# Kernel optimization log

Hardware: AMD Instinct MI355X
Metric: run time of the kernel (lower is better)

## Reference

```python
import jax, jax.numpy as jnp
import numpy as np
from jax import lax

K = 3  # kernel size
KK = K * K


def _bilinear_gather(img, ys, xs):
    """img: [C, H, W]; ys, xs: [KK, H, W] float sample coords.
    Returns [C, KK, H, W], zero outside the image (torch DCN zero-pad semantics)."""
    C, H, W = img.shape
    y0 = jnp.floor(ys).astype(jnp.int32)
    x0 = jnp.floor(xs).astype(jnp.int32)
    y1, x1 = y0 + 1, x0 + 1
    wy1 = ys - y0.astype(ys.dtype)
    wx1 = xs - x0.astype(xs.dtype)
    wy0, wx0 = 1.0 - wy1, 1.0 - wx1

    def g(yi, xi):
        valid = ((yi >= 0) & (yi < H) & (xi >= 0) & (xi < W)).astype(img.dtype)
        yc = jnp.clip(yi, 0, H - 1)
        xc = jnp.clip(xi, 0, W - 1)
        return img[:, yc, xc] * valid[None]  # [C, KK, H, W]

    return (wy0 * wx0) * g(y0, x0) + (wy0 * wx1) * g(y0, x1) \
         + (wy1 * wx0) * g(y1, x0) + (wy1 * wx1) * g(y1, x1)


def _df_layer(x, w_off, b_off, w):
    """One DFConv2d (modulated DCN, k=3, s=1, d=1, pad=1, groups=1) + ReLU."""
    B, C, H, W = x.shape
    O = w.shape[0]
    # offset/mask conv (standard 3x3, pad 1, with bias)
    om = lax.conv_general_dilated(x, w_off, (1, 1), [(1, 1), (1, 1)],
                                  dimension_numbers=('NCHW', 'OIHW', 'NCHW'))
    om = om + b_off[None, :, None, None]                     # [B, 27, H, W]
    off = om[:, :2 * KK].reshape(B, KK, 2, H, W)             # (dy, dx) per kernel pt
    mask = jax.nn.sigmoid(om[:, 2 * KK:3 * KK])              # [B, KK, H, W]

    ki, kj = jnp.meshgrid(jnp.arange(K), jnp.arange(K), indexing='ij')
    # base sampling grid: y = h - pad + i*dil = h + i - 1
    base_y = jnp.arange(H, dtype=x.dtype)[None, :, None] + (ki.reshape(KK, 1, 1).astype(x.dtype) - 1.0)
    base_x = jnp.arange(W, dtype=x.dtype)[None, None, :] + (kj.reshape(KK, 1, 1).astype(x.dtype) - 1.0)
    ys = base_y + off[:, :, 0]                               # [B, KK, H, W]
    xs = base_x + off[:, :, 1]

    sampled = jax.vmap(_bilinear_gather)(x, ys, xs)          # [B, C, KK, H, W]
    out = jnp.einsum('oik,bikhw->bohw', w.reshape(O, C, KK), sampled * mask[:, None])
    return jax.nn.relu(out)


def setup_inputs() -> dict:
    key = jax.random.key(0)
    ks = jax.random.split(key, 7)
    s = 0.05
    return {
        'x': jax.random.normal(ks[0], (2, 256, 96, 96), dtype=jnp.float32),
        'w_off0': jax.random.normal(ks[1], (27, 256, 3, 3), dtype=jnp.float32) * s,
        'b_off0': jnp.zeros((27,), dtype=jnp.float32),
        'w0': jax.random.normal(ks[2], (256, 256, 3, 3), dtype=jnp.float32) * s,
        'w_off1': jax.random.normal(ks[3], (27, 256, 3, 3), dtype=jnp.float32) * s,
        'b_off1': jnp.zeros((27,), dtype=jnp.float32),
        'w1': jax.random.normal(ks[4], (256, 256, 3, 3), dtype=jnp.float32) * s,
    }


def reference(x, w_off0, b_off0, w0, w_off1, b_off1, w1):
    h = _df_layer(x, w_off0, b_off0, w0)
    h = _df_layer(h, w_off1, b_off1, w1)
    return h
```

## Files before the change

### kernel.cpp

```cpp
#include <hip/hip_runtime.h>
#include <cstdint>
#include <cstddef>


#define KTOT 2304
#define PXB  9216

typedef __attribute__((ext_vector_type(8))) short bf16x8;
typedef __attribute__((ext_vector_type(4))) float f32x4;

static __device__ __forceinline__ unsigned short f2bf(float f) {
    union { float f; unsigned int u; } v; v.f = f;
    unsigned int r = (v.u + 0x7FFFu + ((v.u >> 16) & 1u)) >> 16;
    return (unsigned short)r;
}
static __device__ __forceinline__ float bf2f(unsigned short h) {
    union { unsigned int u; float f; } v; v.u = ((unsigned int)h) << 16;
    return v.f;
}
static __device__ __forceinline__ void unpack8(uint4 u, float* f) {
    union { unsigned int u; float f; } t;
    t.u = u.x << 16;         f[0] = t.f;
    t.u = u.x & 0xffff0000u; f[1] = t.f;
    t.u = u.y << 16;         f[2] = t.f;
    t.u = u.y & 0xffff0000u; f[3] = t.f;
    t.u = u.z << 16;         f[4] = t.f;
    t.u = u.z & 0xffff0000u; f[5] = t.f;
    t.u = u.w << 16;         f[6] = t.f;
    t.u = u.w & 0xffff0000u; f[7] = t.f;
}

__global__ __launch_bounds__(256) void transpose_kernel(const float* __restrict__ in,
                                                        unsigned short* __restrict__ outH,
                                                        unsigned short* __restrict__ outL) {
    __shared__ float tile[64][65];
    const int hw0 = blockIdx.x * 64;
    const int c0  = blockIdx.y * 64;
    const int b   = blockIdx.z;
    const int lx  = threadIdx.x & 63;
    const int ly  = threadIdx.x >> 6;
#pragma unroll
    for (int i = 0; i < 16; ++i) {
        int cl = ly + i * 4;
        tile[cl][lx] = in[(size_t)(b * 256 + c0 + cl) * PXB + hw0 + lx];
    }
    __syncthreads();
#pragma unroll
    for (int i = 0; i < 16; ++i) {
        int hwl = ly + i * 4;
        float v = tile[lx][hwl];
        size_t oi = ((size_t)b * PXB + hw0 + hwl) * 256 + c0 + lx;
        unsigned short hi = f2bf(v);
        outH[oi] = hi;
        outL[oi] = f2bf(v - bf2f(hi));
    }
}

__global__ __launch_bounds__(256) void prep_w_kernel(const float* __restrict__ w,
                                                     unsigned short* __restrict__ wA) {
    int idx = blockIdx.x * 256 + threadIdx.x;
    int o = idx / KTOT;
    int k = idx - o * KTOT;
    int kk = k >> 8;
    int c  = k & 255;
    wA[idx] = f2bf(w[o * KTOT + c * 9 + kk]);
}

__global__ __launch_bounds__(256) void prep_woff_kernel(const float* __restrict__ w,
                                                        unsigned short* __restrict__ wH,
                                                        unsigned short* __restrict__ wL) {
    int idx = blockIdx.x * 256 + threadIdx.x;
    int o = idx / KTOT;
    int k = idx - o * KTOT;
    int kk = k >> 8;
    int c  = k & 255;
    float f = (o < 27) ? w[o * KTOT + c * 9 + kk] : 0.0f;
    unsigned short hi = f2bf(f);
    wH[idx] = hi;
    wL[idx] = f2bf(f - bf2f(hi));
}

__global__ __launch_bounds__(512) void offconv_fused(const unsigned short* __restrict__ xH,
                                                     const unsigned short* __restrict__ xL,
                                                     const unsigned short* __restrict__ AH,
                                                     const unsigned short* __restrict__ AL,
                                                     const float* __restrict__ bias,
                                                     float* __restrict__ om) {
    __shared__ __attribute__((aligned(16))) unsigned short AsH[2][32 * 72];
    __shared__ __attribute__((aligned(16))) unsigned short AsL[2][32 * 72];
    __shared__ __attribute__((aligned(16))) unsigned short BsH[2][64 * 72];
    __shared__ __attribute__((aligned(16))) unsigned short BsL[2][64 * 72];

    const int tid  = threadIdx.x;
    const int kg   = tid >> 8;
    const int tl   = tid & 255;
    const int lane = tid & 63;
    const int wq   = (tid >> 6) & 3;
    const int quad = lane >> 4, l16 = lane & 15;
    const int g    = blockIdx.x;
    const int nb   = (g & 7) * 36 + (g >> 3);
    const int n0   = nb * 64;
    const int b    = n0 / PXB;
    const int hw0  = n0 - b * PXB;

    f32x4 acc[2];
#pragma unroll
    for (int mt = 0; mt < 2; ++mt) acc[mt] = (f32x4)0.0f;

    const int arow = tl >> 3, akg = tl & 7;

    uint4 pAH, pAL, pBH0, pBL0, pBH1, pBL1;
    auto pf = [&](int it) {
        const int kt = kg * 18 + it;
        const int kk = kt >> 2, c0 = (kt & 3) * 64;
        const int dy = kk / 3 - 1, dx = kk - (kk / 3) * 3 - 1;
        size_t ai = (size_t)arow * KTOT + kt * 64 + akg * 8;
        pAH = *(const uint4*)&AH[ai];
        pAL = *(const uint4*)&AL[ai];
#pragma unroll
        for (int i = 0; i < 2; ++i) {
            int task = i * 256 + tl;
            int px = task >> 3, cg = task & 7;
            int hw = hw0 + px;
            int h = hw / 96, w = hw - h * 96;
            int y = h + dy, x = w + dx;
            uint4 hv = make_uint4(0u, 0u, 0u, 0u), lv = make_uint4(0u, 0u, 0u, 0u);
            if (((unsigned)y < 96u) && ((unsigned)x < 96u)) {
                size_t bi = ((size_t)b * PXB + y * 96 + x) * 256 + c0 + cg * 8;
                hv = *(const uint4*)&xH[bi];
                lv = *(const uint4*)&xL[bi];
            }
            if (i == 0) { pBH0 = hv; pBL0 = lv; } else { pBH1 = hv; pBL1 = lv; }
        }
    };
    pf(0);

    for (int it = 0; it < 18; ++it) {
        __syncthreads();
        *(uint4*)&AsH[kg][arow * 72 + akg * 8] = pAH;
        *(uint4*)&AsL[kg][arow * 72 + akg * 8] = pAL;
        {
            int px = tl >> 3, cg = tl & 7;
            *(uint4*)&BsH[kg][px * 72 + cg * 8] = pBH0;
            *(uint4*)&BsL[kg][px * 72 + cg * 8] = pBL0;
        }
        {
            int task = 256 + tl;
            int px = task >> 3, cg = task & 7;
            *(uint4*)&BsH[kg][px * 72 + cg * 8] = pBH1;
            *(uint4*)&BsL[kg][px * 72 + cg * 8] = pBL1;
        }
        if (it < 17) pf(it + 1);
        __syncthreads();
#pragma unroll
        for (int ks = 0; ks < 2; ++ks) {
            bf16x8 ah[2], al[2], bh, bl;
#pragma unroll
            for (int mt = 0; mt < 2; ++mt) {
                ah[mt] = *(const bf16x8*)&AsH[kg][(mt * 16 + l16) * 72 + ks * 32 + quad * 8];
                al[mt] = *(const bf16x8*)&AsL[kg][(mt * 16 + l16) * 72 + ks * 32 + quad * 8];
            }
            bh = *(const bf16x8*)&BsH[kg][(wq * 16 + l16) * 72 + ks * 32 + quad * 8];
            bl = *(const bf16x8*)&BsL[kg][(wq * 16 + l16) * 72 + ks * 32 + quad * 8];
#pragma unroll
            for (int mt = 0; mt < 2; ++mt) {
                acc[mt] = __builtin_amdgcn_mfma_f32_16x16x32_bf16(ah[mt], bh, acc[mt], 0, 0, 0);
                acc[mt] = __builtin_amdgcn_mfma_f32_16x16x32_bf16(ah[mt], bl, acc[mt], 0, 0, 0);
                acc[mt] = __builtin_amdgcn_mfma_f32_16x16x32_bf16(al[mt], bh, acc[mt], 0, 0, 0);
            }
        }
    }

    float* red = (float*)BsH;
    __syncthreads();
    if (kg == 1) {
#pragma unroll
        for (int mt = 0; mt < 2; ++mt)
#pragma unroll
            for (int r = 0; r < 4; ++r)
                red[wq * 512 + mt * 256 + quad * 64 + r * 16 + l16] = acc[mt][r];
    }
    __syncthreads();
    if (kg == 0) {
#pragma unroll
        for (int mt = 0; mt < 2; ++mt)
#pragma unroll
            for (int r = 0; r < 4; ++r) {
                float v = acc[mt][r] + red[wq * 512 + mt * 256 + quad * 64 + r * 16 + l16];
                int m = mt * 16 + quad * 4 + r;
                int n = wq * 16 + l16;
                if (m < 27)
                    om[(size_t)(b * 27 + m) * PXB + hw0 + n] = v + bias[m];
            }
    }
}

__global__ __launch_bounds__(512, 4) void dfconv_v2(const unsigned short* __restrict__ xB,
                                                    const float* __restrict__ om,
                                                    const unsigned short* __restrict__ A,
                                                    float* __restrict__ out,
                                                    unsigned short* __restrict__ outH,
                                                    unsigned short* __restrict__ outL,
                                                    int out_mode) {
    __shared__ __attribute__((aligned(16))) char smem[81664];
    unsigned short* Bbuf0 = (unsigned short*)(smem + 65536);
    unsigned short* Bbuf1 = (unsigned short*)(smem + 70144);
    unsigned short* goff  = (unsigned short*)(smem + 74752);
    float*          gwt   = (float*)(smem + 77056);

    const int tid  = threadIdx.x;
    const int wv   = tid >> 6;
    const int lane = tid & 63;
    const int quad = lane >> 4, l16 = lane & 15;
    const int g    = blockIdx.x;
    const int nb   = (g & 7) * 72 + (g >> 3);
    const int n0   = nb * 32;
    const int b    = n0 / PXB;
    const int hw0  = n0 - b * PXB;

    if (tid < 288) {
        int task = tid;
        int px = task / 9;
        int kk = task - px * 9;
        int hw = hw0 + px;
        int h = hw / 96, w = hw - h * 96;
        const float* omp = om + (size_t)b * 27 * PXB + hw;
        float dyv = omp[(size_t)(2 * kk) * PXB];
        float dxv = omp[(size_t)(2 * kk + 1) * PXB];
        float mv  = omp[(size_t)(18 + kk) * PXB];
        float mk  = 1.0f / (1.0f + __expf(-mv));

        float ys = (float)(h + (kk / 3) - 1) + dyv;
        float xs = (float)(w + (kk - (kk / 3) * 3) - 1) + dxv;
        float fy = floorf(ys), fx = floorf(xs);
        int iy = (int)fy, ix = (int)fx;
        float wy1 = ys - fy, wx1 = xs - fx;
        float wy0 = 1.0f - wy1, wx0 = 1.0f - wx1;
        bool yv0 = (unsigned)iy < 96u, yv1 = (unsigned)(iy + 1) < 96u;
        bool xv0 = (unsigned)ix < 96u, xv1 = (unsigned)(ix + 1) < 96u;
        int y0 = min(max(iy, 0), 95),     y1 = min(max(iy + 1, 0), 95);
        int x0 = min(max(ix, 0), 95),     x1 = min(max(ix + 1, 0), 95);
        int gg = task * 4;
        goff[gg + 0] = (unsigned short)(y0 * 96 + x0);
        goff[gg + 1] = (unsigned short)(y0 * 96 + x1);
        goff[gg + 2] = (unsigned short)(y1 * 96 + x0);
        goff[gg + 3] = (unsigned short)(y1 * 96 + x1);
        gwt[gg + 0] = (yv0 && xv0) ? mk * wy0 * wx0 : 0.0f;
        gwt[gg + 1] = (yv0 && xv1) ? mk * wy0 * wx1 : 0.0f;
        gwt[gg + 2] = (yv1 && xv0) ? mk * wy1 * wx0 : 0.0f;
        gwt[gg + 3] = (yv1 && xv1) ? mk * wy1 * wx1 : 0.0f;
    }
    __syncthreads();

    const int px = (tid & 255) >> 3;
    const int cg = tid & 7;
    const unsigned short* xbase = xB + (size_t)b * PXB * 256 + cg * 8;

    const int arl = lane >> 3;
    const int akg = (lane & 7) ^ arl;

    f32x4 acc[2][2];
#pragma unroll
    for (int mt = 0; mt < 2; ++mt)
#pragma unroll
        for (int nt = 0; nt < 2; ++nt) acc[mt][nt] = (f32x4)0.0f;

    auto dmaA = [&](int kt, int buf) {
#pragma unroll
        for (int s = 0; s < 4; ++s) {
            const unsigned short* src =
                A + (size_t)(wv * 32 + s * 8 + arl) * KTOT + kt * 64 + akg * 8;
            char* dst = smem + buf * 32768 + wv * 4096 + s * 1024;
            __builtin_amdgcn_global_load_lds(
                (const __attribute__((address_space(1))) unsigned int*)src,
                (__attribute__((address_space(3))) unsigned int*)dst, 16, 0, 0);
        }
    };

    dmaA(0, 0);
    if (tid < 256) {
        int gg = (px * 9 + 0) * 4;
        ushort4 o4 = *(const ushort4*)&goff[gg];
        float4 wt = *(const float4*)&gwt[gg];
        uint4 u0 = *(const uint4*)(xbase + (size_t)o4.x * 256);
        uint4 u1 = *(const uint4*)(xbase + (size_t)o4.y * 256);
        uint4 u2 = *(const uint4*)(xbase + (size_t)o4.z * 256);
        uint4 u3 = *(const uint4*)(xbase + (size_t)o4.w * 256);
        float f0[8], f1[8], f2[8], f3[8];
        unpack8(u0, f0); unpack8(u1, f1); unpack8(u2, f2); unpack8(u3, f3);
        unsigned short res[8];
#pragma unroll
        for (int j = 0; j < 8; ++j)
            res[j] = f2bf(wt.x * f0[j] + wt.y * f1[j] + wt.z * f2[j] + wt.w * f3[j]);
        *(uint4*)&Bbuf0[px * 72 + cg * 8] = *(uint4*)res;
    }
    __syncthreads();

    for (int r = 0; r < 36; ++r) {
        const int cur = r & 1;

        uint4 cc0, cc1, cc2, cc3; float4 wt;
        if (tid < 256 && r < 35) {
            const int ktn = r + 1, tap = ktn >> 2, c0 = (ktn & 3) * 64;
            int gg = (px * 9 + tap) * 4;
            ushort4 o4 = *(const ushort4*)&goff[gg];
            wt = *(const float4*)&gwt[gg];
            const unsigned short* cb = xbase + c0;
            cc0 = *(const uint4*)(cb + (size_t)o4.x * 256);
            cc1 = *(const uint4*)(cb + (size_t)o4.y * 256);
            cc2 = *(const uint4*)(cb + (size_t)o4.z * 256);
            cc3 = *(const uint4*)(cb + (size_t)o4.w * 256);
        }

        if (r < 35) dmaA(r + 1, cur ^ 1);

        {
            const char* Ac = smem + cur * 32768 + wv * 4096;
            const unsigned short* Br = cur ? Bbuf1 : Bbuf0;
#pragma unroll
            for (int ks = 0; ks < 2; ++ks) {
                const int sw = (((ks * 4 + quad) ^ (l16 & 7)) * 16);
                bf16x8 a0 = *(const bf16x8*)(Ac + l16 * 128 + sw);
                bf16x8 a1 = *(const bf16x8*)(Ac + (16 + l16) * 128 + sw);
                bf16x8 b0 = *(const bf16x8*)&Br[l16 * 72 + ks * 32 + quad * 8];
                bf16x8 b1 = *(const bf16x8*)&Br[(16 + l16) * 72 + ks * 32 + quad * 8];
                acc[0][0] = __builtin_amdgcn_mfma_f32_16x16x32_bf16(a0, b0, acc[0][0], 0, 0, 0);
                acc[0][1] = __builtin_amdgcn_mfma_f32_16x16x32_bf16(a0, b1, acc[0][1], 0, 0, 0);
                acc[1][0] = __builtin_amdgcn_mfma_f32_16x16x32_bf16(a1, b0, acc[1][0], 0, 0, 0);
                acc[1][1] = __builtin_amdgcn_mfma_f32_16x16x32_bf16(a1, b1, acc[1][1], 0, 0, 0);
            }
        }

        if (tid < 256 && r < 35) {
            unsigned short* Bw = cur ? Bbuf0 : Bbuf1;
            float f0[8], f1[8], f2[8], f3[8];
            unpack8(cc0, f0); unpack8(cc1, f1); unpack8(cc2, f2); unpack8(cc3, f3);
            unsigned short res[8];
#pragma unroll
            for (int j = 0; j < 8; ++j)
                res[j] = f2bf(wt.x * f0[j] + wt.y * f1[j] + wt.z * f2[j] + wt.w * f3[j]);
            *(uint4*)&Bw[px * 72 + cg * 8] = *(uint4*)res;
        }

        __syncthreads();
    }

    float* tileS = (float*)smem;
    if (out_mode == 0) {
#pragma unroll
        for (int pass = 0; pass < 2; ++pass) {
            if ((wv >> 2) == pass) {
#pragma unroll
                for (int mt = 0; mt < 2; ++mt)
#pragma unroll
                    for (int nt = 0; nt < 2; ++nt)
#pragma unroll
                        for (int rr = 0; rr < 4; ++rr) {
                            int ml = (wv & 3) * 32 + mt * 16 + quad * 4 + rr;
                            int n  = nt * 16 + l16;
                            tileS[ml * 36 + n] = fmaxf(acc[mt][nt][rr], 0.0f);
                        }
            }
            __syncthreads();
#pragma unroll
            for (int j = 0; j < 2; ++j) {
                int idx = j * 512 + tid;
                int row = idx >> 3, q = idx & 7;
                *(float4*)&out[(size_t)(b * 256 + pass * 128 + row) * PXB + hw0 + q * 4] =
                    *(const float4*)&tileS[row * 36 + q * 4];
            }
            __syncthreads();
        }
    } else {
#pragma unroll
        for (int pass = 0; pass < 2; ++pass) {
#pragma unroll
            for (int mt = 0; mt < 2; ++mt) {
                f32x4 v = acc[mt][pass];
                v[0] = fmaxf(v[0], 0.f); v[1] = fmaxf(v[1], 0.f);
                v[2] = fmaxf(v[2], 0.f); v[3] = fmaxf(v[3], 0.f);
                *(f32x4*)&tileS[l16 * 264 + wv * 32 + mt * 16 + quad * 4] = v;
            }
            __syncthreads();
#pragma unroll
            for (int j = 0; j < 2; ++j) {
                int idx = j * 512 + tid;
                int pxl = idx >> 6, ln = idx & 63;
                float4 v = *(const float4*)&tileS[pxl * 264 + ln * 4];
                size_t oi = ((size_t)b * PXB + hw0 + pass * 16 + pxl) * 256 + ln * 4;
                unsigned short hv[4], lv[4];
#pragma unroll
                for (int e = 0; e < 4; ++e) {
                    float fe = (e == 0) ? v.x : (e == 1) ? v.y : (e == 2) ? v.z : v.w;
                    hv[e] = f2bf(fe);
                    lv[e] = f2bf(fe - bf2f(hv[e]));
                }
                *(ushort4*)&outH[oi] = *(ushort4*)hv;
                *(ushort4*)&outL[oi] = *(ushort4*)lv;
            }
            __syncthreads();
        }
    }
}

extern "C" void kernel_launch(void* const* d_in, const int* in_sizes, int n_in,
                              void* d_out, int out_size, void* d_ws, size_t ws_size,
                              hipStream_t stream) {
    const float* x     = (const float*)d_in[0];
    const float* woff0 = (const float*)d_in[1];
    const float* boff0 = (const float*)d_in[2];
    const float* w0    = (const float*)d_in[3];
    const float* woff1 = (const float*)d_in[4];
    const float* boff1 = (const float*)d_in[5];
    const float* w1    = (const float*)d_in[6];
    float* out = (float*)d_out;

    char* p = (char*)d_ws;
    float* om  = (float*)p;  p += (size_t)2 * 27 * PXB * 4;
    unsigned short* xh  = (unsigned short*)p; p += (size_t)2 * 256 * PXB * 2;
    unsigned short* xl  = (unsigned short*)p; p += (size_t)2 * 256 * PXB * 2;
    unsigned short* h1h = (unsigned short*)p; p += (size_t)2 * 256 * PXB * 2;
    unsigned short* h1l = (unsigned short*)p; p += (size_t)2 * 256 * PXB * 2;
    unsigned short* wA0 = (unsigned short*)p; p += (size_t)256 * KTOT * 2;
    unsigned short* wA1 = (unsigned short*)p; p += (size_t)256 * KTOT * 2;
    unsigned short* wH0 = (unsigned short*)p; p += (size_t)32 * KTOT * 2;
    unsigned short* wL0 = (unsigned short*)p; p += (size_t)32 * KTOT * 2;
    unsigned short* wH1 = (unsigned short*)p; p += (size_t)32 * KTOT * 2;
    unsigned short* wL1 = (unsigned short*)p; p += (size_t)32 * KTOT * 2;

    hipLaunchKernelGGL(transpose_kernel, dim3(PXB / 64, 4, 2), dim3(256), 0, stream, x, xh, xl);
    hipLaunchKernelGGL(prep_w_kernel, dim3(256 * KTOT / 256), dim3(256), 0, stream, w0, wA0);
    hipLaunchKernelGGL(prep_w_kernel, dim3(256 * KTOT / 256), dim3(256), 0, stream, w1, wA1);
    hipLaunchKernelGGL(prep_woff_kernel, dim3(32 * KTOT / 256), dim3(256), 0, stream, woff0, wH0, wL0);
    hipLaunchKernelGGL(prep_woff_kernel, dim3(32 * KTOT / 256), dim3(256), 0, stream, woff1, wH1, wL1);

    hipLaunchKernelGGL(offconv_fused, dim3(288), dim3(512), 0, stream, xh, xl, wH0, wL0, boff0, om);
    hipLaunchKernelGGL(dfconv_v2, dim3(576), dim3(512), 0, stream, xh, om, wA0,
                       (float*)nullptr, h1h, h1l, 1);

    hipLaunchKernelGGL(offconv_fused, dim3(288), dim3(512), 0, stream, h1h, h1l, wH1, wL1, boff1, om);
    hipLaunchKernelGGL(dfconv_v2, dim3(576), dim3(512), 0, stream, h1h, om, wA1,
                       out, (unsigned short*)nullptr, (unsigned short*)nullptr, 0);
}
```

Before: 316.1 us.

## Single-buffer A tile via register prefetch to raise LDS-limited occupancy

The double-buffered LDS tile for the weight matrix A becomes a single buffer. Each wave now loads all of its A fragments for the current k-step into registers and waits for those LDS reads to finish. Only then does it issue the async global-to-LDS DMA for the next k-step into the same per-wave region. This cuts shared memory from about 80KB to about 48KB, and launch bounds go from 4 to 6 so more blocks can be resident per CU. The risks are higher register pressure or spilling under the tighter bound, a serialization point at the lgkmcnt wait, and an epilogue that reuses smem as a float tile and may expect more than the now-smaller buffer.

```diff
diff --git a/kernel.cpp b/kernel.cpp
--- a/kernel.cpp
+++ b/kernel.cpp
@@ -195,18 +195,18 @@
     }
 }
 
-__global__ __launch_bounds__(512, 4) void dfconv_v2(const unsigned short* __restrict__ xB,
+__global__ __launch_bounds__(512, 6) void dfconv_v2(const unsigned short* __restrict__ xB,
                                                     const float* __restrict__ om,
                                                     const unsigned short* __restrict__ A,
                                                     float* __restrict__ out,
                                                     unsigned short* __restrict__ outH,
                                                     unsigned short* __restrict__ outL,
                                                     int out_mode) {
-    __shared__ __attribute__((aligned(16))) char smem[81664];
-    unsigned short* Bbuf0 = (unsigned short*)(smem + 65536);
-    unsigned short* Bbuf1 = (unsigned short*)(smem + 70144);
-    unsigned short* goff  = (unsigned short*)(smem + 74752);
-    float*          gwt   = (float*)(smem + 77056);
+    __shared__ __attribute__((aligned(16))) char smem[48896];
+    unsigned short* Bbuf0 = (unsigned short*)(smem + 32768);
+    unsigned short* Bbuf1 = (unsigned short*)(smem + 37376);
+    unsigned short* goff  = (unsigned short*)(smem + 41984);
+    float*          gwt   = (float*)(smem + 44288);
 
     const int tid  = threadIdx.x;
     const int wv   = tid >> 6;
@@ -265,19 +265,19 @@
 #pragma unroll
         for (int nt = 0; nt < 2; ++nt) acc[mt][nt] = (f32x4)0.0f;
 
-    auto dmaA = [&](int kt, int buf) {
+    auto dmaA = [&](int kt) {
 #pragma unroll
         for (int s = 0; s < 4; ++s) {
             const unsigned short* src =
                 A + (size_t)(wv * 32 + s * 8 + arl) * KTOT + kt * 64 + akg * 8;
-            char* dst = smem + buf * 32768 + wv * 4096 + s * 1024;
+            char* dst = smem + wv * 4096 + s * 1024;
             __builtin_amdgcn_global_load_lds(
                 (const __attribute__((address_space(1))) unsigned int*)src,
                 (__attribute__((address_space(3))) unsigned int*)dst, 16, 0, 0);
         }
     };
 
-    dmaA(0, 0);
+    dmaA(0);
     if (tid < 256) {
         int gg = (px * 9 + 0) * 4;
         ushort4 o4 = *(const ushort4*)&goff[gg];
@@ -312,23 +312,35 @@
             cc3 = *(const uint4*)(cb + (size_t)o4.w * 256);
         }
 
-        if (r < 35) dmaA(r + 1, cur ^ 1);
-
+        bf16x8 af00, af01, af10, af11;
         {
-            const char* Ac = smem + cur * 32768 + wv * 4096;
+            const char* Ac = smem + wv * 4096;
+            const int sw0 = ((quad ^ (l16 & 7)) * 16);
+            const int sw1 = (((4 + quad) ^ (l16 & 7)) * 16);
+            af00 = *(const bf16x8*)(Ac + l16 * 128 + sw0);
+            af01 = *(const bf16x8*)(Ac + (16 + l16) * 128 + sw0);
+            af10 = *(const bf16x8*)(Ac + l16 * 128 + sw1);
+            af11 = *(const bf16x8*)(Ac + (16 + l16) * 128 + sw1);
+        }
+        asm volatile("s_waitcnt lgkmcnt(0)" ::: "memory");
+        __builtin_amdgcn_sched_barrier(0);
+
+        if (r < 35) dmaA(r + 1);
+
+        {
             const unsigned short* Br = cur ? Bbuf1 : Bbuf0;
-#pragma unroll
-            for (int ks = 0; ks < 2; ++ks) {
-                const int sw = (((ks * 4 + quad) ^ (l16 & 7)) * 16);
-                bf16x8 a0 = *(const bf16x8*)(Ac + l16 * 128 + sw);
-                bf16x8 a1 = *(const bf16x8*)(Ac + (16 + l16) * 128 + sw);
-                bf16x8 b0 = *(const bf16x8*)&Br[l16 * 72 + ks * 32 + quad * 8];
-                bf16x8 b1 = *(const bf16x8*)&Br[(16 + l16) * 72 + ks * 32 + quad * 8];
-                acc[0][0] = __builtin_amdgcn_mfma_f32_16x16x32_bf16(a0, b0, acc[0][0], 0, 0, 0);
-                acc[0][1] = __builtin_amdgcn_mfma_f32_16x16x32_bf16(a0, b1, acc[0][1], 0, 0, 0);
-                acc[1][0] = __builtin_amdgcn_mfma_f32_16x16x32_bf16(a1, b0, acc[1][0], 0, 0, 0);
-                acc[1][1] = __builtin_amdgcn_mfma_f32_16x16x32_bf16(a1, b1, acc[1][1], 0, 0, 0);
-            }
+            bf16x8 b0 = *(const bf16x8*)&Br[l16 * 72 + quad * 8];
+            bf16x8 b1 = *(const bf16x8*)&Br[(16 + l16) * 72 + quad * 8];
+            acc[0][0] = __builtin_amdgcn_mfma_f32_16x16x32_bf16(af00, b0, acc[0][0], 0, 0, 0);
+            acc[0][1] = __builtin_amdgcn_mfma_f32_16x16x32_bf16(af00, b1, acc[0][1], 0, 0, 0);
+            acc[1][0] = __builtin_amdgcn_mfma_f32_16x16x32_bf16(af01, b0, acc[1][0], 0, 0, 0);
+            acc[1][1] = __builtin_amdgcn_mfma_f32_16x16x32_bf16(af01, b1, acc[1][1], 0, 0, 0);
+            bf16x8 b2 = *(const bf16x8*)&Br[l16 * 72 + 32 + quad * 8];
+            bf16x8 b3 = *(const bf16x8*)&Br[(16 + l16) * 72 + 32 + quad * 8];
+            acc[0][0] = __builtin_amdgcn_mfma_f32_16x16x32_bf16(af10, b2, acc[0][0], 0, 0, 0);
+            acc[0][1] = __builtin_amdgcn_mfma_f32_16x16x32_bf16(af10, b3, acc[0][1], 0, 0, 0);
+            acc[1][0] = __builtin_amdgcn_mfma_f32_16x16x32_bf16(af11, b2, acc[1][0], 0, 0, 0);
+            acc[1][1] = __builtin_amdgcn_mfma_f32_16x16x32_bf16(af11, b3, acc[1][1], 0, 0, 0);
         }
 
         if (tid < 256 && r < 35) {
```

Result: slower. 395.3 us (+25.1%).

## Double K-step per iteration, single-buffer A in registers, use all threads for gather

Applied to the files above, without the earlier changes.

The deformable conv main loop now handles 128 K per iteration (18 iterations instead of 36). All 512 threads produce bilinear-gathered B tiles, two k-slices at once, instead of only 256. A goes into a single LDS buffer: fragments are read into registers, the loads drain, and then the next A DMA is issued into the same buffer. This halves the barrier count and doubles gather parallelism, but needs more LDS and registers, and launch bounds drop occupancy from 4 to 2 blocks per CU.

```diff
diff --git a/kernel.cpp b/kernel.cpp
--- a/kernel.cpp
+++ b/kernel.cpp
@@ -195,18 +195,17 @@
     }
 }
 
-__global__ __launch_bounds__(512, 4) void dfconv_v2(const unsigned short* __restrict__ xB,
+__global__ __launch_bounds__(512, 2) void dfconv_v3(const unsigned short* __restrict__ xB,
                                                     const float* __restrict__ om,
                                                     const unsigned short* __restrict__ A,
                                                     float* __restrict__ out,
                                                     unsigned short* __restrict__ outH,
                                                     unsigned short* __restrict__ outL,
                                                     int out_mode) {
-    __shared__ __attribute__((aligned(16))) char smem[81664];
-    unsigned short* Bbuf0 = (unsigned short*)(smem + 65536);
-    unsigned short* Bbuf1 = (unsigned short*)(smem + 70144);
-    unsigned short* goff  = (unsigned short*)(smem + 74752);
-    float*          gwt   = (float*)(smem + 77056);
+    __shared__ __attribute__((aligned(16))) char smem[90880];
+    unsigned short* BsD  = (unsigned short*)(smem + 65536);
+    unsigned short* goff = (unsigned short*)(smem + 83968);
+    float*          gwt  = (float*)(smem + 86272);
 
     const int tid  = threadIdx.x;
     const int wv   = tid >> 6;
@@ -252,56 +251,60 @@
     }
     __syncthreads();
 
+    const int p  = tid >> 8;
     const int px = (tid & 255) >> 3;
     const int cg = tid & 7;
     const unsigned short* xbase = xB + (size_t)b * PXB * 256 + cg * 8;
 
-    const int arl = lane >> 3;
-    const int akg = (lane & 7) ^ arl;
-
     f32x4 acc[2][2];
 #pragma unroll
     for (int mt = 0; mt < 2; ++mt)
 #pragma unroll
         for (int nt = 0; nt < 2; ++nt) acc[mt][nt] = (f32x4)0.0f;
 
-    auto dmaA = [&](int kt, int buf) {
-#pragma unroll
-        for (int s = 0; s < 4; ++s) {
+    const int rsh = lane >> 4;
+    const int slt = lane & 15;
+    auto dmaA = [&](int r) {
+#pragma unroll
+        for (int s = 0; s < 8; ++s) {
+            const int row = s * 4 + rsh;
+            const int gs  = slt ^ (row & 15);
             const unsigned short* src =
-                A + (size_t)(wv * 32 + s * 8 + arl) * KTOT + kt * 64 + akg * 8;
-            char* dst = smem + buf * 32768 + wv * 4096 + s * 1024;
+                A + (size_t)(wv * 32 + row) * KTOT + r * 128 + gs * 8;
+            char* dst = smem + wv * 8192 + s * 1024;
             __builtin_amdgcn_global_load_lds(
                 (const __attribute__((address_space(1))) unsigned int*)src,
                 (__attribute__((address_space(3))) unsigned int*)dst, 16, 0, 0);
         }
     };
 
-    dmaA(0, 0);
-    if (tid < 256) {
-        int gg = (px * 9 + 0) * 4;
+    dmaA(0);
+    {
+        const int kt = p, tap = kt >> 2, c0 = (kt & 3) * 64;
+        int gg = (px * 9 + tap) * 4;
         ushort4 o4 = *(const ushort4*)&goff[gg];
         float4 wt = *(const float4*)&gwt[gg];
-        uint4 u0 = *(const uint4*)(xbase + (size_t)o4.x * 256);
-        uint4 u1 = *(const uint4*)(xbase + (size_t)o4.y * 256);
-        uint4 u2 = *(const uint4*)(xbase + (size_t)o4.z * 256);
-        uint4 u3 = *(const uint4*)(xbase + (size_t)o4.w * 256);
+        const unsigned short* cb = xbase + c0;
+        uint4 u0 = *(const uint4*)(cb + (size_t)o4.x * 256);
+        uint4 u1 = *(const uint4*)(cb + (size_t)o4.y * 256);
+        uint4 u2 = *(const uint4*)(cb + (size_t)o4.z * 256);
+        uint4 u3 = *(const uint4*)(cb + (size_t)o4.w * 256);
         float f0[8], f1[8], f2[8], f3[8];
         unpack8(u0, f0); unpack8(u1, f1); unpack8(u2, f2); unpack8(u3, f3);
         unsigned short res[8];
 #pragma unroll
         for (int j = 0; j < 8; ++j)
             res[j] = f2bf(wt.x * f0[j] + wt.y * f1[j] + wt.z * f2[j] + wt.w * f3[j]);
-        *(uint4*)&Bbuf0[px * 72 + cg * 8] = *(uint4*)res;
+        *(uint4*)&BsD[p * 2304 + px * 72 + cg * 8] = *(uint4*)res;
     }
     __syncthreads();
 
-    for (int r = 0; r < 36; ++r) {
+    for (int r = 0; r < 18; ++r) {
         const int cur = r & 1;
 
         uint4 cc0, cc1, cc2, cc3; float4 wt;
-        if (tid < 256 && r < 35) {
-            const int ktn = r + 1, tap = ktn >> 2, c0 = (ktn & 3) * 64;
+        if (r < 17) {
+            const int ktn = 2 * (r + 1) + p, tap = ktn >> 2, c0 = (ktn & 3) * 64;
             int gg = (px * 9 + tap) * 4;
             ushort4 o4 = *(const ushort4*)&goff[gg];
             wt = *(const float4*)&gwt[gg];
@@ -312,27 +315,42 @@
             cc3 = *(const uint4*)(cb + (size_t)o4.w * 256);
         }
 
-        if (r < 35) dmaA(r + 1, cur ^ 1);
-
+        bf16x8 af[2][2][2];
         {
-            const char* Ac = smem + cur * 32768 + wv * 4096;
-            const unsigned short* Br = cur ? Bbuf1 : Bbuf0;
+            const char* Ac = smem + wv * 8192;
+#pragma unroll
+            for (int pp = 0; pp < 2; ++pp)
+#pragma unroll
+                for (int ks = 0; ks < 2; ++ks)
+#pragma unroll
+                    for (int mt = 0; mt < 2; ++mt) {
+                        const int row = mt * 16 + l16;
+                        const int gw  = pp * 8 + ks * 4 + quad;
+                        af[pp][ks][mt] = *(const bf16x8*)(Ac + row * 256
+                                                          + ((gw ^ (row & 15)) * 16));
+                    }
+        }
+        asm volatile("s_waitcnt lgkmcnt(0)" ::: "memory");
+        __builtin_amdgcn_sched_barrier(0);
+
+        if (r < 17) dmaA(r + 1);
+
+#pragma unroll
+        for (int pp = 0; pp < 2; ++pp) {
+            const unsigned short* Br = BsD + (cur * 2 + pp) * 2304;
 #pragma unroll
             for (int ks = 0; ks < 2; ++ks) {
-                const int sw = (((ks * 4 + quad) ^ (l16 & 7)) * 16);
-                bf16x8 a0 = *(const bf16x8*)(Ac + l16 * 128 + sw);
-                bf16x8 a1 = *(const bf16x8*)(Ac + (16 + l16) * 128 + sw);
                 bf16x8 b0 = *(const bf16x8*)&Br[l16 * 72 + ks * 32 + quad * 8];
                 bf16x8 b1 = *(const bf16x8*)&Br[(16 + l16) * 72 + ks * 32 + quad * 8];
-                acc[0][0] = __builtin_amdgcn_mfma_f32_16x16x32_bf16(a0, b0, acc[0][0], 0, 0, 0);
-                acc[0][1] = __builtin_amdgcn_mfma_f32_16x16x32_bf16(a0, b1, acc[0][1], 0, 0, 0);
-                acc[1][0] = __builtin_amdgcn_mfma_f32_16x16x32_bf16(a1, b0, acc[1][0], 0, 0, 0);
-                acc[1][1] = __builtin_amdgcn_mfma_f32_16x16x32_bf16(a1, b1, acc[1][1], 0, 0, 0);
-            }
-        }
-
-        if (tid < 256 && r < 35) {
-            unsigned short* Bw = cur ? Bbuf0 : Bbuf1;
+                acc[0][0] = __builtin_amdgcn_mfma_f32_16x16x32_bf16(af[pp][ks][0], b0, acc[0][0], 0, 0, 0);
+                acc[0][1] = __builtin_amdgcn_mfma_f32_16x16x32_bf16(af[pp][ks][0], b1, acc[0][1], 0, 0, 0);
+                acc[1][0] = __builtin_amdgcn_mfma_f32_16x16x32_bf16(af[pp][ks][1], b0, acc[1][0], 0, 0, 0);
+                acc[1][1] = __builtin_amdgcn_mfma_f32_16x16x32_bf16(af[pp][ks][1], b1, acc[1][1], 0, 0, 0);
+            }
+        }
+
+        if (r < 17) {
+            unsigned short* Bw = BsD + ((cur ^ 1) * 2 + p) * 2304;
             float f0[8], f1[8], f2[8], f3[8];
             unpack8(cc0, f0); unpack8(cc1, f1); unpack8(cc2, f2); unpack8(cc3, f3);
             unsigned short res[8];
@@ -435,10 +453,10 @@
     hipLaunchKernelGGL(prep_woff_kernel, dim3(32 * KTOT / 256), dim3(256), 0, stream, woff1, wH1, wL1);
 
     hipLaunchKernelGGL(offconv_fused, dim3(288), dim3(512), 0, stream, xh, xl, wH0, wL0, boff0, om);
-    hipLaunchKernelGGL(dfconv_v2, dim3(576), dim3(512), 0, stream, xh, om, wA0,
+    hipLaunchKernelGGL(dfconv_v3, dim3(576), dim3(512), 0, stream, xh, om, wA0,
                        (float*)nullptr, h1h, h1l, 1);
 
     hipLaunchKernelGGL(offconv_fused, dim3(288), dim3(512), 0, stream, h1h, h1l, wH1, wL1, boff1, om);
-    hipLaunchKernelGGL(dfconv_v2, dim3(576), dim3(512), 0, stream, h1h, om, wA1,
+    hipLaunchKernelGGL(dfconv_v3, dim3(576), dim3(512), 0, stream, h1h, om, wA1,
                        out, (unsigned short*)nullptr, (unsigned short*)nullptr, 0);
 }
```

Result: slower. 346.3 us (+9.6%).
